# Optimization experiments

Measured on AMD Instinct MI355X. Metric: run time of the kernel, lower is better.

The kernel has to match this reference:

```python
import jax, jax.numpy as jnp
import numpy as np

N_E, N_IN = 1024, 64
HIDDEN, OUT = 128, 64


def setup_inputs() -> dict:
    key = jax.random.key(0)
    kx, k1, k2 = jax.random.split(key, 3)
    x = jax.random.normal(kx, (N_E, N_IN), dtype=jnp.float32)
    # edge-MLP params: Dense(2*n_in -> HIDDEN) + tanh + Dense(HIDDEN -> OUT)
    W1 = jax.random.normal(k1, (2 * N_IN, HIDDEN), dtype=jnp.float32) / np.sqrt(2 * N_IN)
    b1 = jnp.zeros((HIDDEN,), dtype=jnp.float32)
    W2 = jax.random.normal(k2, (HIDDEN, OUT), dtype=jnp.float32) / np.sqrt(HIDDEN)
    b2 = jnp.zeros((OUT,), dtype=jnp.float32)
    return {"x": x, "W1": W1, "b1": b1, "W2": W2, "b2": b2}


def reference(x, W1, b1, W2, b2):
    n_e, n_in = x.shape
    # modular all-pairs index: partner of i is (i + j) % n_e for j in 1..n_e-1
    pair_idx = (jnp.arange(n_e)[:, None] + jnp.arange(1, n_e)[None, :]) % n_e  # [n_e, n_e-1]
    # pairs[i, j] = concat(x[i], x[pair_idx[i, j]])  -> [n_e, n_e-1, 2*n_in]
    self_feat = jnp.broadcast_to(x[:, None, :], (n_e, n_e - 1, n_in))
    pairs = jnp.concatenate([self_feat, x[pair_idx]], axis=-1)
    # edge MLP: Dense + tanh + Dense
    h = jnp.tanh(jnp.einsum("epf,fh->eph", pairs, W1) + b1)
    upd = jnp.einsum("eph,ho->epo", h, W2) + b2
    # mean over partners
    return jnp.mean(upd, axis=1)  # [n_e, OUT]
```

## Files before the change

kernel.cpp:

```cpp
#include <hip/hip_runtime.h>


#define N_E  1024
#define NIN  64
#define HID  128
#define OUTD 64
#define PCH  30
#define NQ   32
#define S_CH 5.5f

static constexpr float INV_S     = 1.0f / 5.5f;
static constexpr float TWO_LOG2E = 2.8853900817779268f;
static constexpr float PI_F      = 3.14159265358979323846f;

__device__ __forceinline__ float tanh_fast(float u) {
  return 1.0f - 2.0f * __builtin_amdgcn_rcpf(
      1.0f + __builtin_amdgcn_exp2f(u * TWO_LOG2E));
}

__global__ __launch_bounds__(256) void prep_coeff_kernel(
    const float* __restrict__ x, const float* __restrict__ W1,
    const float* __restrict__ b1,
    float* __restrict__ A, float* __restrict__ B,
    float* __restrict__ C, float* __restrict__ M) {
  const int t = threadIdx.x;
  if (blockIdx.x < N_E / 2) {
    __shared__ float xs[2][NIN];
    const int sub = t >> 7, h = t & (HID - 1);
    const int i = blockIdx.x * 2 + sub;
    if (t < 2 * NIN) xs[t >> 6][t & 63] = x[(blockIdx.x * 2 + (t >> 6)) * NIN + (t & 63)];
    __syncthreads();
    float accA = 0.f, accB = 0.f;
    #pragma unroll 8
    for (int f = 0; f < NIN; ++f) {
      const float xv = xs[sub][f];
      accA += xv * W1[f * HID + h];
      accB += xv * W1[(NIN + f) * HID + h];
    }
    A[i * HID + h] = accA;
    B[i * HID + h] = accB + b1[h];
  } else {
    __shared__ float ctab[NQ + 1];
    __shared__ float fg[(NQ + 1) * (NQ + 2)];
    __shared__ float G[PCH * (NQ + 2)];
    if (t <= NQ) ctab[t] = cosf((float)t * (PI_F / (float)NQ));
    for (int idx = t; idx < PCH * HID; idx += 256) M[idx] = 0.f;
    __syncthreads();
    for (int idx = t; idx < (NQ + 1) * (NQ + 1); idx += 256) {
      const int j = idx / (NQ + 1), l = idx % (NQ + 1);
      fg[j * (NQ + 2) + l] = tanh_fast(S_CH * (ctab[j] + ctab[l]));
    }
    __syncthreads();
    for (int idx = t; idx < PCH * (NQ + 1); idx += 256) {
      const int q = idx / (NQ + 1), j = idx % (NQ + 1);
      const float cphi = ctab[q];
      float c0 = 1.f, c1 = cphi;
      float s = 0.5f * fg[j * (NQ + 2) + 0];
      for (int l = 1; l <= NQ; ++l) {
        const float w = (l == NQ) ? 0.5f : 1.0f;
        s += w * fg[j * (NQ + 2) + l] * c1;
        const float c2 = 2.f * cphi * c1 - c0; c0 = c1; c1 = c2;
      }
      G[q * (NQ + 2) + j] = s;
    }
    __syncthreads();
    for (int idx = t; idx < PCH * PCH; idx += 256) {
      const int p = idx / PCH, q = idx % PCH;
      const float cphi = ctab[p];
      float c0 = 1.f, c1 = cphi;
      float s = 0.5f * G[q * (NQ + 2) + 0];
      for (int j = 1; j <= NQ; ++j) {
        const float w = (j == NQ) ? 0.5f : 1.0f;
        s += w * G[q * (NQ + 2) + j] * c1;
        const float c2 = 2.f * cphi * c1 - c0; c0 = c1; c1 = c2;
      }
      const float cp = (p == 0 ? 1.f : 2.f) / (float)NQ;
      const float cq = (q == 0 ? 1.f : 2.f) / (float)NQ;
      C[p * PCH + q] = s * cp * cq;
    }
  }
}

__global__ __launch_bounds__(256) void moments_kernel(
    const float* __restrict__ B, float* __restrict__ M) {
  __shared__ float Msub[PCH][256];
  const int t = threadIdx.x;
  const int h = t & (HID - 1), sub = t >> 7;
  float acc[PCH];
  #pragma unroll
  for (int q = 0; q < PCH; ++q) acc[q] = 0.f;
  const int k0 = blockIdx.x * 16 + sub * 8;
  for (int j = 0; j < 8; ++j) {
    float b = B[(k0 + j) * HID + h];
    b = fminf(fmaxf(b, -S_CH), S_CH) * INV_S;
    float t0 = 1.f, t1 = b;
    const float b2x = b + b;
    acc[0] += 1.f;
    acc[1] += b;
    #pragma unroll
    for (int q = 2; q < PCH; ++q) {
      const float t2 = b2x * t1 - t0;
      acc[q] += t2;
      t0 = t1; t1 = t2;
    }
  }
  #pragma unroll
  for (int q = 0; q < PCH; ++q) Msub[q][t] = acc[q];
  __syncthreads();
  for (int idx = t; idx < PCH * HID; idx += 256) {
    const int q = idx / HID, hh = idx % HID;
    atomicAdd(&M[q * HID + hh], Msub[q][hh] + Msub[q][hh + HID]);
  }
}

__global__ __launch_bounds__(HID) void v_kernel(
    const float* __restrict__ C, const float* __restrict__ M,
    float* __restrict__ V) {
  const int p = blockIdx.x, h = threadIdx.x;
  float acc = 0.f;
  #pragma unroll
  for (int q = 0; q < PCH; ++q) acc += C[p * PCH + q] * M[q * HID + h];
  V[p * HID + h] = acc;
}

__global__ __launch_bounds__(HID) void combine_out_kernel(
    const float* __restrict__ A, const float* __restrict__ B,
    const float* __restrict__ V, const float* __restrict__ W2,
    const float* __restrict__ b2, float* __restrict__ out) {
  __shared__ float Sl[HID];
  __shared__ float red[2][OUTD];
  const int i = blockIdx.x, h = threadIdx.x;
  const float ar = A[i * HID + h], br = B[i * HID + h];
  const float a = fminf(fmaxf(ar, -S_CH), S_CH) * INV_S;
  float t0 = 1.f, t1 = a;
  const float a2x = a + a;
  float acc = V[h] + a * V[HID + h];
  #pragma unroll
  for (int p = 2; p < PCH; ++p) {
    const float t2 = a2x * t1 - t0;
    acc += t2 * V[p * HID + h];
    t0 = t1; t1 = t2;
  }
  const float ts = tanh_fast(ar + br);
  Sl[h] = (acc - ts) * (1.f / (float)(N_E - 1));
  __syncthreads();
  const int o = h & (OUTD - 1), half = h >> 6;
  const int h0 = half * 64;
  float po = 0.f;
  #pragma unroll 16
  for (int hh = 0; hh < 64; ++hh)
    po += Sl[h0 + hh] * W2[(h0 + hh) * OUTD + o];
  red[half][o] = po;
  __syncthreads();
  if (h < OUTD) out[i * OUTD + h] = red[0][h] + red[1][h] + b2[h];
}

extern "C" void kernel_launch(void* const* d_in, const int* in_sizes, int n_in,
                              void* d_out, int out_size, void* d_ws, size_t ws_size,
                              hipStream_t stream) {
  const float* x  = (const float*)d_in[0];
  const float* W1 = (const float*)d_in[1];
  const float* b1 = (const float*)d_in[2];
  const float* W2 = (const float*)d_in[3];
  const float* b2 = (const float*)d_in[4];
  float* out = (float*)d_out;

  float* A = (float*)d_ws;
  float* B = A + N_E * HID;
  float* M = B + N_E * HID;
  float* V = M + PCH * HID;
  float* C = V + PCH * HID;

  prep_coeff_kernel<<<N_E / 2 + 1, 256, 0, stream>>>(x, W1, b1, A, B, C, M);
  moments_kernel<<<N_E / 16, 256, 0, stream>>>(B, M);
  v_kernel<<<PCH, HID, 0, stream>>>(C, M, V);
  combine_out_kernel<<<N_E, HID, 0, stream>>>(A, B, V, W2, b2, out);
}
```

Measured before the change: 76.35 us.

## Fuse V computation into combine kernel and process four rows per block

Removes the separate v_kernel launch by having every combine block recompute V = C·M into shared memory, split across two thread halves. Each 256-thread block now handles four output rows instead of one, so the W2 matvec runs over 256 outputs per block with float4 shared reads. This drops one kernel launch and the V round trip through global memory. The cost is redundant per-block V recomputation of roughly 30x30x128 FMAs and more register pressure from the v[30] array.

Result: no change. 76.92 us (+0.7%).

```diff
diff --git a/kernel.cpp b/kernel.cpp
--- a/kernel.cpp
+++ b/kernel.cpp
@@ -109,50 +109,69 @@
   __syncthreads();
   for (int idx = t; idx < PCH * HID; idx += 256) {
     const int q = idx / HID, hh = idx % HID;
-    atomicAdd(&M[q * HID + hh], Msub[q][hh] + Msub[q][hh + HID]);
+    atomicAdd(&M[idx], Msub[q][hh] + Msub[q][hh + HID]);
   }
 }
 
-__global__ __launch_bounds__(HID) void v_kernel(
+__global__ __launch_bounds__(256) void combine_out_kernel(
+    const float* __restrict__ A, const float* __restrict__ B,
     const float* __restrict__ C, const float* __restrict__ M,
-    float* __restrict__ V) {
-  const int p = blockIdx.x, h = threadIdx.x;
-  float acc = 0.f;
+    const float* __restrict__ W2, const float* __restrict__ b2,
+    float* __restrict__ out) {
+  const int t = threadIdx.x;
+  const int h = t & (HID - 1), sub = t >> 7;
+  __shared__ float Vs[2][PCH][HID];
+  __shared__ float Sl[4][HID];
+
+  float m[PCH / 2];
   #pragma unroll
-  for (int q = 0; q < PCH; ++q) acc += C[p * PCH + q] * M[q * HID + h];
-  V[p * HID + h] = acc;
-}
+  for (int qq = 0; qq < PCH / 2; ++qq)
+    m[qq] = M[(sub * (PCH / 2) + qq) * HID + h];
+  #pragma unroll
+  for (int p = 0; p < PCH; ++p) {
+    float s = 0.f;
+    #pragma unroll
+    for (int qq = 0; qq < PCH / 2; ++qq)
+      s += C[p * PCH + sub * (PCH / 2) + qq] * m[qq];
+    Vs[sub][p][h] = s;
+  }
+  __syncthreads();
+  float v[PCH];
+  #pragma unroll
+  for (int p = 0; p < PCH; ++p) v[p] = Vs[0][p][h] + Vs[1][p][h];
 
-__global__ __launch_bounds__(HID) void combine_out_kernel(
-    const float* __restrict__ A, const float* __restrict__ B,
-    const float* __restrict__ V, const float* __restrict__ W2,
-    const float* __restrict__ b2, float* __restrict__ out) {
-  __shared__ float Sl[HID];
-  __shared__ float red[2][OUTD];
-  const int i = blockIdx.x, h = threadIdx.x;
-  const float ar = A[i * HID + h], br = B[i * HID + h];
-  const float a = fminf(fmaxf(ar, -S_CH), S_CH) * INV_S;
-  float t0 = 1.f, t1 = a;
-  const float a2x = a + a;
-  float acc = V[h] + a * V[HID + h];
   #pragma unroll
-  for (int p = 2; p < PCH; ++p) {
-    const float t2 = a2x * t1 - t0;
-    acc += t2 * V[p * HID + h];
-    t0 = t1; t1 = t2;
+  for (int r = 0; r < 2; ++r) {
+    const int i = blockIdx.x * 4 + sub * 2 + r;
+    const float ar = A[i * HID + h];
+    const float br = B[i * HID + h];
+    const float ua = fminf(fmaxf(ar, -S_CH), S_CH) * INV_S;
+    float s = v[0] + ua * v[1];
+    float t0 = 1.f, t1 = ua;
+    const float ua2 = ua + ua;
+    #pragma unroll
+    for (int p = 2; p < PCH; ++p) {
+      const float t2 = ua2 * t1 - t0;
+      s += t2 * v[p];
+      t0 = t1; t1 = t2;
+    }
+    const float self = tanh_fast(ar + br);
+    Sl[sub * 2 + r][h] = (s - self) * (1.0f / (float)(N_E - 1));
   }
-  const float ts = tanh_fast(ar + br);
-  Sl[h] = (acc - ts) * (1.f / (float)(N_E - 1));
   __syncthreads();
-  const int o = h & (OUTD - 1), half = h >> 6;
-  const int h0 = half * 64;
-  float po = 0.f;
-  #pragma unroll 16
-  for (int hh = 0; hh < 64; ++hh)
-    po += Sl[h0 + hh] * W2[(h0 + hh) * OUTD + o];
-  red[half][o] = po;
-  __syncthreads();
-  if (h < OUTD) out[i * OUTD + h] = red[0][h] + red[1][h] + b2[h];
+  const int o = t & (OUTD - 1), r4 = t >> 6;
+  const float4* __restrict__ slr = (const float4*)&Sl[r4][0];
+  float accO = b2[o];
+  #pragma unroll
+  for (int hh4 = 0; hh4 < HID / 4; ++hh4) {
+    const float4 sv = slr[hh4];
+    const int hb = hh4 * 4;
+    accO += sv.x * W2[(hb + 0) * OUTD + o];
+    accO += sv.y * W2[(hb + 1) * OUTD + o];
+    accO += sv.z * W2[(hb + 2) * OUTD + o];
+    accO += sv.w * W2[(hb + 3) * OUTD + o];
+  }
+  out[blockIdx.x * 256 + t] = accO;
 }
 
 extern "C" void kernel_launch(void* const* d_in, const int* in_sizes, int n_in,
@@ -168,11 +187,9 @@
   float* A = (float*)d_ws;
   float* B = A + N_E * HID;
   float* M = B + N_E * HID;
-  float* V = M + PCH * HID;
-  float* C = V + PCH * HID;
+  float* C = M + PCH * HID;
 
   prep_coeff_kernel<<<N_E / 2 + 1, 256, 0, stream>>>(x, W1, b1, A, B, C, M);
   moments_kernel<<<N_E / 16, 256, 0, stream>>>(B, M);
-  v_kernel<<<PCH, HID, 0, stream>>>(C, M, V);
-  combine_out_kernel<<<N_E, HID, 0, stream>>>(A, B, V, W2, b2, out);
+  combine_out_kernel<<<N_E / 4, 256, 0, stream>>>(A, B, C, M, W2, b2, out);
 }
```
